# Performance work log

Measured on AMD Instinct MI355X. Metric: run time of the kernel, lower is better.

Reference implementation:

```python
import jax, jax.numpy as jnp
import numpy as np

SQUARE_SIZE = 32
BATCH, CH, H, W = 256, 3, 224, 224


def setup_inputs() -> dict:
    key = jax.random.key(0)
    k1, k2, k3 = jax.random.split(key, 3)
    img = jax.random.normal(k1, (BATCH, CH, H, W), dtype=jnp.float32)
    hi = H - SQUARE_SIZE + 1  # 193
    y_idx = jax.random.randint(k2, (BATCH,), 0, hi, dtype=jnp.int32)
    x_idx = jax.random.randint(k3, (BATCH,), 0, hi, dtype=jnp.int32)
    return {"img": img, "y_idx": y_idx, "x_idx": x_idx}


def reference(img, y_idx, x_idx):
    # img: [B, C, H, W]; y_idx/x_idx: [B] top-left corners of zeroed square.
    B, C, H, W = img.shape
    rows = jnp.arange(H, dtype=jnp.int32)  # [H]
    cols = jnp.arange(W, dtype=jnp.int32)  # [W]
    # in_y: [B, H], in_x: [B, W]
    in_y = (rows[None, :] >= y_idx[:, None]) & (rows[None, :] < y_idx[:, None] + SQUARE_SIZE)
    in_x = (cols[None, :] >= x_idx[:, None]) & (cols[None, :] < x_idx[:, None] + SQUARE_SIZE)
    # square region -> mask 0, else 1; broadcast over channels
    in_square = in_y[:, None, :, None] & in_x[:, None, None, :]  # [B, 1, H, W]
    mask = jnp.where(in_square, jnp.float32(0.0), jnp.float32(1.0))
    return img * mask
```

## Files before the change

### kernel.cpp

```cpp
#include <hip/hip_runtime.h>


#define SQ 32
#define B_ 256
#define C_ 3
#define H_ 224
#define W_ 224

__global__ __launch_bounds__(256) void rsd_kernel(const float4* __restrict__ img,
                                                  const int* __restrict__ y_idx,
                                                  const int* __restrict__ x_idx,
                                                  float4* __restrict__ out,
                                                  int total4) {
    int i4 = blockIdx.x * 256 + threadIdx.x;
    if (i4 >= total4) return;

    float4 v = img[i4];

    int i = i4 << 2;
    int w = i % W_;
    int t = i / W_;
    int h = t % H_;
    int b = t / (C_ * H_);

    int y0 = y_idx[b];
    int x0 = x_idx[b];

    bool row_in = (h >= y0) & (h < y0 + SQ);
    if (row_in) {
        if ((w + 0) >= x0 && (w + 0) < x0 + SQ) v.x = 0.0f;
        if ((w + 1) >= x0 && (w + 1) < x0 + SQ) v.y = 0.0f;
        if ((w + 2) >= x0 && (w + 2) < x0 + SQ) v.z = 0.0f;
        if ((w + 3) >= x0 && (w + 3) < x0 + SQ) v.w = 0.0f;
    }

    out[i4] = v;
}

extern "C" void kernel_launch(void* const* d_in, const int* in_sizes, int n_in,
                              void* d_out, int out_size, void* d_ws, size_t ws_size,
                              hipStream_t stream) {
    const float4* img  = (const float4*)d_in[0];
    const int*    yidx = (const int*)d_in[1];
    const int*    xidx = (const int*)d_in[2];
    float4*       out  = (float4*)d_out;

    int total4 = out_size / 4;
    int blocks = (total4 + 255) / 256;
    rsd_kernel<<<blocks, 256, 0, stream>>>(img, yidx, xidx, out, total4);
}
```

Baseline: 255.8 us.

## Replace masked elementwise kernel with device memcpy plus small square-zeroing kernel

The full-image masked copy is replaced by a device-to-device hipMemcpyAsync of the input into the output, followed by a small kernel that writes zeros only into each image's 32x32x3 square. The aim is to use the runtime's copy engine or optimized copy path for the bulk traffic and drop the per-element index arithmetic. It adds a second launch and an ordering dependency, and the memcpy path may be slower than a tuned vectorized kernel.

```diff
diff --git a/kernel.cpp b/kernel.cpp
--- a/kernel.cpp
+++ b/kernel.cpp
@@ -7,45 +7,33 @@
 #define H_ 224
 #define W_ 224
 
-__global__ __launch_bounds__(256) void rsd_kernel(const float4* __restrict__ img,
-                                                  const int* __restrict__ y_idx,
-                                                  const int* __restrict__ x_idx,
-                                                  float4* __restrict__ out,
-                                                  int total4) {
-    int i4 = blockIdx.x * 256 + threadIdx.x;
-    if (i4 >= total4) return;
+__global__ __launch_bounds__(256) void zero_squares(float* __restrict__ out,
+                                                    const int* __restrict__ y_idx,
+                                                    const int* __restrict__ x_idx) {
+    const int b  = (int)blockIdx.x;
+    const int y0 = y_idx[b];
+    const int x0 = x_idx[b];
+    const int t  = (int)threadIdx.x;
 
-    float4 v = img[i4];
-
-    int i = i4 << 2;
-    int w = i % W_;
-    int t = i / W_;
-    int h = t % H_;
-    int b = t / (C_ * H_);
-
-    int y0 = y_idx[b];
-    int x0 = x_idx[b];
-
-    bool row_in = (h >= y0) & (h < y0 + SQ);
-    if (row_in) {
-        if ((w + 0) >= x0 && (w + 0) < x0 + SQ) v.x = 0.0f;
-        if ((w + 1) >= x0 && (w + 1) < x0 + SQ) v.y = 0.0f;
-        if ((w + 2) >= x0 && (w + 2) < x0 + SQ) v.z = 0.0f;
-        if ((w + 3) >= x0 && (w + 3) < x0 + SQ) v.w = 0.0f;
+#pragma unroll
+    for (int e = t; e < C_ * SQ * SQ; e += 256) {
+        const int c = e >> 10;
+        const int r = (e >> 5) & 31;
+        const int x = e & 31;
+        out[((b * C_ + c) * H_ + (y0 + r)) * W_ + (x0 + x)] = 0.0f;
     }
-
-    out[i4] = v;
 }
 
 extern "C" void kernel_launch(void* const* d_in, const int* in_sizes, int n_in,
                               void* d_out, int out_size, void* d_ws, size_t ws_size,
                               hipStream_t stream) {
-    const float4* img  = (const float4*)d_in[0];
-    const int*    yidx = (const int*)d_in[1];
-    const int*    xidx = (const int*)d_in[2];
-    float4*       out  = (float4*)d_out;
+    const void* img  = d_in[0];
+    const int*  yidx = (const int*)d_in[1];
+    const int*  xidx = (const int*)d_in[2];
 
-    int total4 = out_size / 4;
-    int blocks = (total4 + 255) / 256;
-    rsd_kernel<<<blocks, 256, 0, stream>>>(img, yidx, xidx, out, total4);
+    const size_t nbytes = (size_t)out_size * sizeof(float);
+
+    hipMemcpyAsync(d_out, img, nbytes, hipMemcpyDeviceToDevice, stream);
+
+    zero_squares<<<dim3(B_), 256, 0, stream>>>((float*)d_out, yidx, xidx);
 }
```

After: 267.2 us. 4.5% more time.
